# Kernel optimization log

Hardware: AMD Instinct MI355X
Metric: run time of the kernel (lower is better)

## Reference

```python
import jax, jax.numpy as jnp
from jax import lax
import numpy as np

B, T, L, N, H, DI, DO = 1024, 512, 64, 8, 128, 32, 16
STEPS, MULT = 64, 8  # real_indices = arange(STEPS)*MULT


def setup_inputs() -> dict:
    key = jax.random.key(0)
    ks = jax.random.split(key, 16)
    w = lambda k, s: jax.random.normal(k, s, jnp.float32) * 0.01  # nn.init.normal_(std=0.01)
    z = lambda s: jnp.zeros(s, jnp.float32)
    return {
        "init_noise": jax.random.normal(ks[0], (B, DI), jnp.float32),
        "dw_noise": jax.random.normal(ks[1], (T - 1, B, N), jnp.float32),  # standard normal, scaled by sqrt(dt) inside
        "ts": jnp.arange(T, dtype=jnp.float32) / (T - 1),  # sde_times_full on [0, 1]
        "emb_W": w(ks[2], (DI, L)), "emb_b": z((L,)),
        "f_W1": w(ks[3], (L + 1, H)), "f_b1": z((H,)),
        "f_W2": w(ks[4], (H, H)), "f_b2": z((H,)),
        "f_W3": w(ks[5], (H, L)), "f_b3": z((L,)),
        "g_W1": w(ks[6], (L + 1, H)), "g_b1": z((H,)),
        "g_W2": w(ks[7], (H, H)), "g_b2": z((H,)),
        "g_W3": w(ks[8], (H, L * N)), "g_b3": z((L * N,)),
        "r_W1": w(ks[9], (L, H)), "r_b1": z((H,)),
        "r_W2": w(ks[10], (H, DO)), "r_b2": z((DO,)),
    }


def _tz_mlp(t, zb, W1, b1, W2, b2, W3, b3):
    tz = jnp.concatenate([jnp.full((zb.shape[0], 1), t, zb.dtype), zb], axis=-1)
    h = jax.nn.softplus(tz @ W1 + b1)
    h = jax.nn.softplus(h @ W2 + b2)
    return jnp.tanh(h @ W3 + b3)


def reference(init_noise, dw_noise, ts, emb_W, emb_b,
              f_W1, f_b1, f_W2, f_b2, f_W3, f_b3,
              g_W1, g_b1, g_W2, g_b2, g_W3, g_b3,
              r_W1, r_b1, r_W2, r_b2):
    z0 = init_noise @ emb_W + emb_b  # (B, L)
    dt = ts[1:] - ts[:-1]  # (T-1,)
    dW = dw_noise * jnp.sqrt(dt)[:, None, None]  # Brownian increments (T-1, B, N)

    def step(zc, xs):
        t, dti, dwi = xs
        f = _tz_mlp(t, zc, f_W1, f_b1, f_W2, f_b2, f_W3, f_b3)  # (B, L) drift
        g = _tz_mlp(t, zc, g_W1, g_b1, g_W2, g_b2, g_W3, g_b3).reshape(zc.shape[0], L, N)
        zn = zc + f * dti + jnp.einsum('bln,bn->bl', g, dwi)  # Euler-Maruyama (ito)
        return zn, zn

    _, zs = lax.scan(step, z0, (ts[:-1], dt, dW))  # (T-1, B, L)
    z_path = jnp.concatenate([z0[None], zs], axis=0).transpose(1, 0, 2)  # (B, T, L)

    x_hat_full = jax.nn.relu(z_path @ r_W1 + r_b1) @ r_W2 + r_b2  # (B, T, DO)
    real_indices = jnp.arange(STEPS) * MULT
    x_hat_matched = x_hat_full[:, real_indices, :]  # (B, STEPS, DO)
    return x_hat_full, x_hat_matched
```

## Files before the change

kernel.cpp:

```cpp
#include <hip/hip_runtime.h>
#include <cmath>


typedef _Float16 half8 __attribute__((ext_vector_type(8)));
typedef float floatx4 __attribute__((ext_vector_type(4)));

#define H_FW1 0
#define H_GW1 8192
#define H_FW2 16384
#define H_GW2 32768
#define H_FW3 49152
#define H_GW3 57344
#define H_RW1 122880
#define H_RW2 131072
#define H_TOTAL 133120
#define F_EMBT 66560
#define F_W1R0F (F_EMBT + 2048)
#define F_W1R0G (F_W1R0F + 128)
#define F_CNT 2304
#define PREP_TOTAL (H_TOTAL + F_CNT)

__global__ void prep_kernel(const float* __restrict__ fW1, const float* __restrict__ gW1,
                            const float* __restrict__ fW2, const float* __restrict__ gW2,
                            const float* __restrict__ fW3, const float* __restrict__ gW3,
                            const float* __restrict__ rW1, const float* __restrict__ rW2,
                            const float* __restrict__ embW, void* __restrict__ ws) {
  int idx = blockIdx.x * blockDim.x + threadIdx.x;
  if (idx >= PREP_TOTAL) return;
  if (idx < H_TOTAL) {
    float v;
    if (idx < H_GW1) {
      int t = idx; int c = t >> 6, k = t & 63; v = fW1[(k + 1) * 128 + c];
    } else if (idx < H_FW2) {
      int t = idx - H_GW1; int c = t >> 6, k = t & 63; v = gW1[(k + 1) * 128 + c];
    } else if (idx < H_GW2) {
      int t = idx - H_FW2; int c = t >> 7, k = t & 127; v = fW2[k * 128 + c];
    } else if (idx < H_FW3) {
      int t = idx - H_GW2; int c = t >> 7, k = t & 127; v = gW2[k * 128 + c];
    } else if (idx < H_GW3) {
      int t = idx - H_FW3; int c = t >> 7, k = t & 127; v = fW3[k * 64 + c];
    } else if (idx < H_RW1) {
      int t = idx - H_GW3; int c = t >> 7, k = t & 127; v = gW3[k * 512 + c];
    } else if (idx < H_RW2) {
      int t = idx - H_RW1; int c = t >> 6, k = t & 63; v = rW1[k * 128 + c];
    } else {
      int t = idx - H_RW2; int c = t >> 7, k = t & 127; v = rW2[k * 16 + c];
    }
    ((_Float16*)ws)[idx] = (_Float16)v;
  } else {
    int f = idx - H_TOTAL;
    float v;
    if (f < 2048) {
      int c = f >> 5, k = f & 31; v = embW[k * 64 + c];
      ((float*)ws)[F_EMBT + f] = v;
    } else if (f < 2176) {
      ((float*)ws)[F_W1R0F + (f - 2048)] = fW1[f - 2048];
    } else {
      ((float*)ws)[F_W1R0G + (f - 2176)] = gW1[f - 2176];
    }
  }
}

__device__ __forceinline__ float sp(float x) { return __logf(1.f + __expf(x)); }

__device__ __forceinline__ float ftanh(float x) {
  float e = __expf(2.f * x);
  return 1.f - __fdividef(2.f, e + 1.f);
}

__device__ __forceinline__ floatx4 mfma16(half8 a, half8 b, floatx4 c) {
  return __builtin_amdgcn_mfma_f32_16x16x32_f16(a, b, c, 0, 0, 0);
}

__device__ __forceinline__ int aofs2(int m, int k) {
  int subk = (k >> 3) & 3;
  return ((k >> 5) << 9) + (subk << 7) + ((subk & 1) << 5) + (m << 3) + (k & 7);
}

__device__ __forceinline__ float qsel(floatx4 c, int quad) {
  float v01 = (quad & 1) ? c[1] : c[0];
  float v23 = (quad & 1) ? c[3] : c[2];
  return (quad & 2) ? v23 : v01;
}

#define BAR()                                                    \
  do {                                                           \
    asm volatile("s_waitcnt lgkmcnt(0)" ::: "memory");           \
    __builtin_amdgcn_s_barrier();                                \
    asm volatile("" ::: "memory");                               \
  } while (0)

__global__ __launch_bounds__(512, 2)
void sde_main(const float* __restrict__ init_noise, const float* __restrict__ dw_noise,
              const float* __restrict__ emb_b,
              const float* __restrict__ f_b1, const float* __restrict__ f_b2,
              const float* __restrict__ f_b3, const float* __restrict__ g_b1,
              const float* __restrict__ g_b2, const float* __restrict__ g_b3,
              const float* __restrict__ r_b1, const float* __restrict__ r_b2,
              const void* __restrict__ ws, float* __restrict__ out_full,
              float* __restrict__ out_match) {
  __shared__ __align__(16) _Float16 zseg[1024];
  __shared__ __align__(16) _Float16 h1f[2048], h1g[2048];
  __shared__ __align__(16) _Float16 h2f[2048], h2g[2048];
  __shared__ __align__(16) _Float16 hrsg[2048];
  __shared__ __align__(16) float fps[4 * 80];
  __shared__ __align__(16) float gps[4 * 532];
  __shared__ __align__(16) float zb[4 * 68];
  __shared__ __align__(16) float dwS[2][4][12];

  const int tid = threadIdx.x;
  const int w = tid >> 6;
  const int lane = tid & 63;
  const int ln16 = lane & 15;
  const int quad = lane >> 4;
  const int koff = quad * 8;
  const int wm = w & 3;
  const int b4 = blockIdx.x << 2;
  const _Float16* wsh = (const _Float16*)ws;
  const float* wsf = (const float*)ws;

  const float DTI = 1.0f / 511.0f;
  const float SDT = sqrtf(DTI);

  const int col1 = w * 16 + ln16;
  const float b1fv = f_b1[col1], b1gv = g_b1[col1];
  const float w1fv = wsf[F_W1R0F + col1], w1gv = wsf[F_W1R0G + col1];
  const float rb1v = r_b1[col1];
  const int colA = wm * 32 + ln16, colB = colA + 16;
  const float* bsrc2 = (w < 4) ? f_b2 : g_b2;
  const float b2vA = bsrc2[colA], b2vB = bsrc2[colB];
  const int ra = ((lane >> 4) << 7) + (((lane >> 4) & 1) << 5) + ((lane & 3) << 3);
  const int haddr1 = aofs2(quad, col1);
  const int haddr2A = aofs2(quad, colA), haddr2B = aofs2(quad, colB);
  const int gpsbase = quad * 532 + w * 64 + ln16;
  const int fpsaddr = quad * 80 + (w & 3) * 16 + ln16;
  const int odd = tid & 1, hh = tid >> 1;
  const int rr4 = hh & 3, l4 = hh >> 2, o4 = odd * 4;
  const int gofs = rr4 * 532 + l4 * 8 + o4;
  const int dwofs = rr4 * 12 + o4;
  const int zwaddr = aofs2(rr4, l4);
  const int zbofs = rr4 * 68 + l4;
  const float fbv = f_b3[l4];
  const float4 gbv4 = *(const float4*)(&g_b3[l4 * 8 + o4]);
  const float rb2v = r_b2[ln16];
  const size_t ofull4 = ((size_t)(b4 + quad) * 512) * 16 + ln16;
  const size_t omatch4 = ((size_t)(b4 + quad) * 64) * 16 + ln16;

  if (tid < 128) gps[(tid >> 5) * 532 + (tid & 31)] = init_noise[b4 * 32 + tid];
  if (w == 7 && lane < 32)
    dwS[0][lane >> 3][lane & 7] = dw_noise[b4 * 8 + lane] * SDT;

  half8 Bf1[2], Bg1[2], Br1[2], B2[2][4], B3g[4][4], U3[4];
#pragma unroll
  for (int kf = 0; kf < 2; ++kf) {
    Bf1[kf] = *(const half8*)(wsh + H_FW1 + col1 * 64 + kf * 32 + koff);
    Bg1[kf] = *(const half8*)(wsh + H_GW1 + col1 * 64 + kf * 32 + koff);
    Br1[kf] = *(const half8*)(wsh + H_RW1 + col1 * 64 + kf * 32 + koff);
  }
  const _Float16* w2b = wsh + (w < 4 ? H_FW2 : H_GW2);
#pragma unroll
  for (int i2 = 0; i2 < 2; ++i2)
#pragma unroll
    for (int kf = 0; kf < 4; ++kf)
      B2[i2][kf] = *(const half8*)(w2b + ((wm * 2 + i2) * 16 + ln16) * 128 + kf * 32 + koff);
#pragma unroll
  for (int i2 = 0; i2 < 4; ++i2)
#pragma unroll
    for (int kf = 0; kf < 4; ++kf)
      B3g[i2][kf] = *(const half8*)(wsh + H_GW3 + ((w * 4 + i2) * 16 + ln16) * 128 + kf * 32 + koff);
  {
    const _Float16* u3b = (w < 4) ? (wsh + H_FW3 + (wm * 16 + ln16) * 128)
                                  : (wsh + H_RW2 + ln16 * 128);
#pragma unroll
    for (int kf = 0; kf < 4; ++kf)
      U3[kf] = *(const half8*)(u3b + kf * 32 + koff);
  }
  __syncthreads();

  if (tid < 256) {
    const int rr = tid & 3, l = tid >> 2;
    const float* pe = wsf + F_EMBT + l * 32;
    float acc = emb_b[l];
#pragma unroll
    for (int c = 0; c < 8; ++c) {
      float4 a = *(const float4*)(&gps[rr * 532 + 4 * c]);
      float4 v = *(const float4*)(pe + 4 * c);
      acc += a.x * v.x + a.y * v.y + a.z * v.z + a.w * v.w;
    }
    zb[rr * 68 + l] = acc;
    zseg[aofs2(rr, l)] = (_Float16)acc;
  }
  __syncthreads();

  float zreg = odd ? 0.f : zb[zbofs];

  float dwn = 0.f;

#pragma unroll 1
  for (int i = 0; i < 511; ++i) {
    const float t_s = (float)i * DTI;

    {
      half8 a0 = *(const half8*)(&zseg[ra]);
      half8 a1 = *(const half8*)(&zseg[512 + ra]);
      if (w == 7 && lane < 32) {
        int ip = (i < 510) ? i + 1 : 510;
        dwn = dw_noise[(size_t)ip * 8192 + b4 * 8 + lane];
      }
      floatx4 cf = {0.f, 0.f, 0.f, 0.f}, cg = {0.f, 0.f, 0.f, 0.f}, cr = {0.f, 0.f, 0.f, 0.f};
      cf = mfma16(a0, Bf1[0], cf); cf = mfma16(a1, Bf1[1], cf);
      cg = mfma16(a0, Bg1[0], cg); cg = mfma16(a1, Bg1[1], cg);
      cr = mfma16(a0, Br1[0], cr); cr = mfma16(a1, Br1[1], cr);
      float vf = qsel(cf, quad), vg = qsel(cg, quad), vr = qsel(cr, quad);
      h1f[haddr1] = (_Float16)sp(vf + b1fv + t_s * w1fv);
      h1g[haddr1] = (_Float16)sp(vg + b1gv + t_s * w1gv);
      hrsg[haddr1] = (_Float16)fmaxf(vr + rb1v, 0.f);
    }
    BAR();

    {
      const _Float16* asrc = (w < 4) ? h1f : h1g;
      half8 a[4];
#pragma unroll
      for (int s = 0; s < 4; ++s) a[s] = *(const half8*)(&asrc[s * 512 + ra]);
      floatx4 c0 = {0.f, 0.f, 0.f, 0.f}, c1 = {0.f, 0.f, 0.f, 0.f};
#pragma unroll
      for (int s = 0; s < 4; ++s) {
        c0 = mfma16(a[s], B2[0][s], c0);
        c1 = mfma16(a[s], B2[1][s], c1);
      }
      if (w == 4) {
        half8 hr[4];
#pragma unroll
        for (int s = 0; s < 4; ++s) hr[s] = *(const half8*)(&hrsg[s * 512 + ra]);
        floatx4 co = {0.f, 0.f, 0.f, 0.f};
#pragma unroll
        for (int s = 0; s < 4; ++s) co = mfma16(hr[s], U3[s], co);
        float v = qsel(co, quad) + rb2v;
        out_full[ofull4 + (size_t)i * 16] = v;
        if ((i & 7) == 0) out_match[omatch4 + (size_t)(i >> 3) * 16] = v;
      }
      if (w == 7 && lane < 32)
        dwS[(i + 1) & 1][lane >> 3][lane & 7] = dwn * SDT;
      _Float16* dst = (w < 4) ? h2f : h2g;
      float v0 = qsel(c0, quad), v1 = qsel(c1, quad);
      dst[haddr2A] = (_Float16)sp(v0 + b2vA);
      dst[haddr2B] = (_Float16)sp(v1 + b2vB);
    }
    BAR();

    {
      half8 ag[4];
#pragma unroll
      for (int s = 0; s < 4; ++s) ag[s] = *(const half8*)(&h2g[s * 512 + ra]);
      floatx4 cg4[4];
#pragma unroll
      for (int i2 = 0; i2 < 4; ++i2) cg4[i2] = (floatx4){0.f, 0.f, 0.f, 0.f};
#pragma unroll
      for (int s = 0; s < 4; ++s)
#pragma unroll
        for (int i2 = 0; i2 < 4; ++i2) cg4[i2] = mfma16(ag[s], B3g[i2][s], cg4[i2]);
      floatx4 cf3 = {0.f, 0.f, 0.f, 0.f};
      if (w < 4) {
#pragma unroll
        for (int s = 0; s < 4; ++s) {
          half8 af = *(const half8*)(&h2f[s * 512 + ra]);
          cf3 = mfma16(af, U3[s], cf3);
        }
      }
#pragma unroll
      for (int i2 = 0; i2 < 4; ++i2)
        gps[gpsbase + i2 * 16] = qsel(cg4[i2], quad);
      if (w < 4) fps[fpsaddr] = qsel(cf3, quad);
    }
    BAR();

    {
      const float* dwp = &dwS[0][0][0] + 48 * (i & 1);
      float4 dv = *(const float4*)(dwp + dwofs);
      float4 g = *(const float4*)(&gps[gofs]);
      float acc = ftanh(g.x + gbv4.x) * dv.x
                + ftanh(g.y + gbv4.y) * dv.y
                + ftanh(g.z + gbv4.z) * dv.z
                + ftanh(g.w + gbv4.w) * dv.w;
      if (!odd) acc += ftanh(fps[rr4 * 80 + l4] + fbv) * DTI;
      acc += __shfl_xor(acc, 1);
      if (!odd) {
        zreg += acc;
        zseg[zwaddr] = (_Float16)zreg;
      }
    }
    BAR();
  }

  {
    half8 a0 = *(const half8*)(&zseg[ra]);
    half8 a1 = *(const half8*)(&zseg[512 + ra]);
    floatx4 cr = {0.f, 0.f, 0.f, 0.f};
    cr = mfma16(a0, Br1[0], cr); cr = mfma16(a1, Br1[1], cr);
    float vr = qsel(cr, quad);
    hrsg[haddr1] = (_Float16)fmaxf(vr + rb1v, 0.f);
  }
  BAR();
  if (w == 4) {
    half8 hr[4];
#pragma unroll
    for (int s = 0; s < 4; ++s) hr[s] = *(const half8*)(&hrsg[s * 512 + ra]);
    floatx4 co = {0.f, 0.f, 0.f, 0.f};
#pragma unroll
    for (int s = 0; s < 4; ++s) co = mfma16(hr[s], U3[s], co);
    float v = qsel(co, quad) + rb2v;
    out_full[ofull4 + (size_t)511 * 16] = v;
  }
}

extern "C" void kernel_launch(void* const* d_in, const int* in_sizes, int n_in,
                              void* d_out, int out_size, void* d_ws, size_t ws_size,
                              hipStream_t stream) {
  (void)in_sizes; (void)n_in; (void)out_size; (void)ws_size;
  const float* init_noise = (const float*)d_in[0];
  const float* dw_noise   = (const float*)d_in[1];
  const float* emb_W      = (const float*)d_in[3];
  const float* emb_b      = (const float*)d_in[4];
  const float* f_W1       = (const float*)d_in[5];
  const float* f_b1       = (const float*)d_in[6];
  const float* f_W2       = (const float*)d_in[7];
  const float* f_b2       = (const float*)d_in[8];
  const float* f_W3       = (const float*)d_in[9];
  const float* f_b3       = (const float*)d_in[10];
  const float* g_W1       = (const float*)d_in[11];
  const float* g_b1       = (const float*)d_in[12];
  const float* g_W2       = (const float*)d_in[13];
  const float* g_b2       = (const float*)d_in[14];
  const float* g_W3       = (const float*)d_in[15];
  const float* g_b3       = (const float*)d_in[16];
  const float* r_W1       = (const float*)d_in[17];
  const float* r_b1       = (const float*)d_in[18];
  const float* r_W2       = (const float*)d_in[19];
  const float* r_b2       = (const float*)d_in[20];
  float* out_full = (float*)d_out;
  float* out_match = out_full + (size_t)1024 * 512 * 16;

  hipLaunchKernelGGL(prep_kernel, dim3((PREP_TOTAL + 255) / 256), dim3(256), 0, stream,
                     f_W1, g_W1, f_W2, g_W2, f_W3, g_W3, r_W1, r_W2, emb_W, d_ws);
  hipLaunchKernelGGL(sde_main, dim3(256), dim3(512), 0, stream,
                     init_noise, dw_noise, emb_b, f_b1, f_b2, f_b3,
                     g_b1, g_b2, g_b3, r_b1, r_b2, d_ws, out_full, out_match);
}
```

Measured before the change: 957.9 us.

## Fuse SDE update into layer-3 phase with register shuffles, dropping a barrier

Each wave now computes the f layer-3 output redundantly, applies tanh and the noise scaling in registers, and reduces the g·dW contraction with cross-lane xor shuffles instead of staging partial products through shared memory. This removes the gps/fps LDS round-trip and one block barrier per time step out of three. In exchange, all 8 waves run the f layer-3 MFMAs, more tanh work and many shuffles, and the W3/RW2 fragments need extra registers (R2W added).

```diff
diff --git a/kernel.cpp b/kernel.cpp
--- a/kernel.cpp
+++ b/kernel.cpp
@@ -83,6 +83,12 @@
   return (quad & 2) ? v23 : v01;
 }
 
+__device__ __forceinline__ float sel4(float v0, float v1, float v2, float v3, int s) {
+  float a = (s & 1) ? v1 : v0;
+  float b = (s & 1) ? v3 : v2;
+  return (s & 2) ? b : a;
+}
+
 #define BAR()                                                    \
   do {                                                           \
     asm volatile("s_waitcnt lgkmcnt(0)" ::: "memory");           \
@@ -103,10 +109,9 @@
   __shared__ __align__(16) _Float16 h1f[2048], h1g[2048];
   __shared__ __align__(16) _Float16 h2f[2048], h2g[2048];
   __shared__ __align__(16) _Float16 hrsg[2048];
-  __shared__ __align__(16) float fps[4 * 80];
-  __shared__ __align__(16) float gps[4 * 532];
   __shared__ __align__(16) float zb[4 * 68];
   __shared__ __align__(16) float dwS[2][4][12];
+  __shared__ __align__(16) float stg[4 * 36];
 
   const int tid = threadIdx.x;
   const int w = tid >> 6;
@@ -132,25 +137,28 @@
   const int ra = ((lane >> 4) << 7) + (((lane >> 4) & 1) << 5) + ((lane & 3) << 3);
   const int haddr1 = aofs2(quad, col1);
   const int haddr2A = aofs2(quad, colA), haddr2B = aofs2(quad, colB);
-  const int gpsbase = quad * 532 + w * 64 + ln16;
-  const int fpsaddr = quad * 80 + (w & 3) * 16 + ln16;
-  const int odd = tid & 1, hh = tid >> 1;
-  const int rr4 = hh & 3, l4 = hh >> 2, o4 = odd * 4;
-  const int gofs = rr4 * 532 + l4 * 8 + o4;
-  const int dwofs = rr4 * 12 + o4;
-  const int zwaddr = aofs2(rr4, l4);
-  const int zbofs = rr4 * 68 + l4;
-  const float fbv = f_b3[l4];
-  const float4 gbv4 = *(const float4*)(&g_b3[l4 * 8 + o4]);
+  const int n8 = ln16 & 7;
+  const int hlf = ln16 >> 3;
+  const bool writer = ((n8 & 1) == hlf);
+  const int lstar = (w << 3) + n8;
+  const int i2sel = n8 >> 1;
+  const int fsrc = quad * 16 + ((w & 1) << 3) + n8;
+  const int zwaddr = aofs2(quad, lstar);
+  const int fcol = ((w >> 1) << 4) + ln16;
+  const float fb3v = f_b3[fcol];
+  const float gb0 = g_b3[w * 64 + 0 * 16 + ln16];
+  const float gb1 = g_b3[w * 64 + 1 * 16 + ln16];
+  const float gb2 = g_b3[w * 64 + 2 * 16 + ln16];
+  const float gb3v = g_b3[w * 64 + 3 * 16 + ln16];
   const float rb2v = r_b2[ln16];
   const size_t ofull4 = ((size_t)(b4 + quad) * 512) * 16 + ln16;
   const size_t omatch4 = ((size_t)(b4 + quad) * 64) * 16 + ln16;
 
-  if (tid < 128) gps[(tid >> 5) * 532 + (tid & 31)] = init_noise[b4 * 32 + tid];
+  if (tid < 128) stg[(tid >> 5) * 36 + (tid & 31)] = init_noise[b4 * 32 + tid];
   if (w == 7 && lane < 32)
     dwS[0][lane >> 3][lane & 7] = dw_noise[b4 * 8 + lane] * SDT;
 
-  half8 Bf1[2], Bg1[2], Br1[2], B2[2][4], B3g[4][4], U3[4];
+  half8 Bf1[2], Bg1[2], Br1[2], B2[2][4], B3g[4][4], U3[4], R2W[4];
 #pragma unroll
   for (int kf = 0; kf < 2; ++kf) {
     Bf1[kf] = *(const half8*)(wsh + H_FW1 + col1 * 64 + kf * 32 + koff);
@@ -168,12 +176,10 @@
 #pragma unroll
     for (int kf = 0; kf < 4; ++kf)
       B3g[i2][kf] = *(const half8*)(wsh + H_GW3 + ((w * 4 + i2) * 16 + ln16) * 128 + kf * 32 + koff);
-  {
-    const _Float16* u3b = (w < 4) ? (wsh + H_FW3 + (wm * 16 + ln16) * 128)
-                                  : (wsh + H_RW2 + ln16 * 128);
-#pragma unroll
-    for (int kf = 0; kf < 4; ++kf)
-      U3[kf] = *(const half8*)(u3b + kf * 32 + koff);
+#pragma unroll
+  for (int kf = 0; kf < 4; ++kf) {
+    U3[kf] = *(const half8*)(wsh + H_FW3 + fcol * 128 + kf * 32 + koff);
+    R2W[kf] = *(const half8*)(wsh + H_RW2 + ln16 * 128 + kf * 32 + koff);
   }
   __syncthreads();
 
@@ -183,7 +189,7 @@
     float acc = emb_b[l];
 #pragma unroll
     for (int c = 0; c < 8; ++c) {
-      float4 a = *(const float4*)(&gps[rr * 532 + 4 * c]);
+      float4 a = *(const float4*)(&stg[rr * 36 + 4 * c]);
       float4 v = *(const float4*)(pe + 4 * c);
       acc += a.x * v.x + a.y * v.y + a.z * v.z + a.w * v.w;
     }
@@ -192,7 +198,7 @@
   }
   __syncthreads();
 
-  float zreg = odd ? 0.f : zb[zbofs];
+  float zreg = writer ? zb[quad * 68 + lstar] : 0.f;
 
   float dwn = 0.f;
 
@@ -235,7 +241,7 @@
         for (int s = 0; s < 4; ++s) hr[s] = *(const half8*)(&hrsg[s * 512 + ra]);
         floatx4 co = {0.f, 0.f, 0.f, 0.f};
 #pragma unroll
-        for (int s = 0; s < 4; ++s) co = mfma16(hr[s], U3[s], co);
+        for (int s = 0; s < 4; ++s) co = mfma16(hr[s], R2W[s], co);
         float v = qsel(co, quad) + rb2v;
         out_full[ofull4 + (size_t)i * 16] = v;
         if ((i & 7) == 0) out_match[omatch4 + (size_t)(i >> 3) * 16] = v;
@@ -261,32 +267,25 @@
 #pragma unroll
         for (int i2 = 0; i2 < 4; ++i2) cg4[i2] = mfma16(ag[s], B3g[i2][s], cg4[i2]);
       floatx4 cf3 = {0.f, 0.f, 0.f, 0.f};
-      if (w < 4) {
-#pragma unroll
-        for (int s = 0; s < 4; ++s) {
-          half8 af = *(const half8*)(&h2f[s * 512 + ra]);
-          cf3 = mfma16(af, U3[s], cf3);
-        }
-      }
-#pragma unroll
-      for (int i2 = 0; i2 < 4; ++i2)
-        gps[gpsbase + i2 * 16] = qsel(cg4[i2], quad);
-      if (w < 4) fps[fpsaddr] = qsel(cf3, quad);
-    }
-    BAR();
-
-    {
-      const float* dwp = &dwS[0][0][0] + 48 * (i & 1);
-      float4 dv = *(const float4*)(dwp + dwofs);
-      float4 g = *(const float4*)(&gps[gofs]);
-      float acc = ftanh(g.x + gbv4.x) * dv.x
-                + ftanh(g.y + gbv4.y) * dv.y
-                + ftanh(g.z + gbv4.z) * dv.z
-                + ftanh(g.w + gbv4.w) * dv.w;
-      if (!odd) acc += ftanh(fps[rr4 * 80 + l4] + fbv) * DTI;
-      acc += __shfl_xor(acc, 1);
-      if (!odd) {
-        zreg += acc;
+#pragma unroll
+      for (int s = 0; s < 4; ++s) {
+        half8 af = *(const half8*)(&h2f[s * 512 + ra]);
+        cf3 = mfma16(af, U3[s], cf3);
+      }
+      float dwv = dwS[i & 1][quad][n8];
+      float ft = ftanh(qsel(cf3, quad) + fb3v) * DTI;
+      float v0 = ftanh(qsel(cg4[0], quad) + gb0) * dwv;
+      float v1 = ftanh(qsel(cg4[1], quad) + gb1) * dwv;
+      float v2 = ftanh(qsel(cg4[2], quad) + gb2) * dwv;
+      float v3 = ftanh(qsel(cg4[3], quad) + gb3v) * dwv;
+      v0 += __shfl_xor(v0, 1); v0 += __shfl_xor(v0, 2); v0 += __shfl_xor(v0, 4);
+      v1 += __shfl_xor(v1, 1); v1 += __shfl_xor(v1, 2); v1 += __shfl_xor(v1, 4);
+      v2 += __shfl_xor(v2, 1); v2 += __shfl_xor(v2, 2); v2 += __shfl_xor(v2, 4);
+      v3 += __shfl_xor(v3, 1); v3 += __shfl_xor(v3, 2); v3 += __shfl_xor(v3, 4);
+      float ftl = __shfl(ft, fsrc);
+      float S = sel4(v0, v1, v2, v3, i2sel);
+      if (writer) {
+        zreg += S + ftl;
         zseg[zwaddr] = (_Float16)zreg;
       }
     }
@@ -308,7 +307,7 @@
     for (int s = 0; s < 4; ++s) hr[s] = *(const half8*)(&hrsg[s * 512 + ra]);
     floatx4 co = {0.f, 0.f, 0.f, 0.f};
 #pragma unroll
-    for (int s = 0; s < 4; ++s) co = mfma16(hr[s], U3[s], co);
+    for (int s = 0; s < 4; ++s) co = mfma16(hr[s], R2W[s], co);
     float v = qsel(co, quad) + rb2v;
     out_full[ofull4 + (size_t)511 * 16] = v;
   }
```

Result: no change. 948.5 us (-1.0%).
